# Kernel tuning notes

Measured on AMD Instinct MI355X. Metric: run time of the kernel, lower is better.

The kernel has to match this reference:

```python
import jax, jax.numpy as jnp
import numpy as np

N, T, D, H, P = 4096, 365, 16, 256, 2


def setup_inputs() -> dict:
    key = jax.random.key(0)
    ks = jax.random.split(key, 16)
    std = 0.02
    inputs = jax.random.normal(ks[0], (N, T, D), dtype=jnp.float32)
    A = jax.random.uniform(ks[1], (N, N), dtype=jnp.float32)
    A = A / jnp.sum(A, axis=1, keepdims=True)  # row-normalized adjacency
    return {
        "inputs": inputs,
        "A": A,
        # Keras LSTMCell params: kernel [D,4H], recurrent_kernel [H,4H], bias [4H]
        "kernel": jax.random.normal(ks[2], (D, 4 * H), dtype=jnp.float32) * std,
        "rkernel": jax.random.normal(ks[3], (H, 4 * H), dtype=jnp.float32) * std,
        "lstm_bias": jnp.zeros((4 * H,), dtype=jnp.float32),
        "W_graph_h": jax.random.normal(ks[4], (H, H), dtype=jnp.float32) * std,
        "b_graph_h": jnp.zeros((H,), dtype=jnp.float32),
        "W_graph_c": jax.random.normal(ks[5], (H, H), dtype=jnp.float32) * std,
        "b_graph_c": jnp.zeros((H,), dtype=jnp.float32),
        "W_h_cur": jax.random.normal(ks[6], (H, H), dtype=jnp.float32) * std,
        "W_h_prev": jax.random.normal(ks[7], (H, H), dtype=jnp.float32) * std,
        "b_h": jnp.zeros((H,), dtype=jnp.float32),
        "W_c_cur": jax.random.normal(ks[8], (H, H), dtype=jnp.float32) * std,
        "W_c_prev": jax.random.normal(ks[9], (H, H), dtype=jnp.float32) * std,
        "b_c": jnp.zeros((H,), dtype=jnp.float32),
        "W_out": jax.random.normal(ks[10], (H, P), dtype=jnp.float32) * std,
        "b_out": jnp.zeros((P,), dtype=jnp.float32),
    }


def reference(inputs, A, kernel, rkernel, lstm_bias,
              W_graph_h, b_graph_h, W_graph_c, b_graph_c,
              W_h_cur, W_h_prev, b_h, W_c_cur, W_c_prev, b_c,
              W_out, b_out):
    h = A.shape[0] and None  # noop; shapes: inputs [N,T,D]
    n = A.shape[0]
    hs = W_graph_h.shape[0]

    def step(carry, x_t):
        h_prev, c_prev = carry  # [N,H] each
        # graph propagation of previous states
        h_graph = jnp.tanh(A @ (h_prev @ W_graph_h + b_graph_h))
        c_graph = jnp.tanh(A @ (c_prev @ W_graph_c + b_graph_c))
        # Keras LSTMCell (gate order i, f, g, o)
        z = x_t @ kernel + h_prev @ rkernel + lstm_bias  # [N,4H]
        zi, zf, zg, zo = jnp.split(z, 4, axis=-1)
        c_cur = jax.nn.sigmoid(zf) * c_prev + jax.nn.sigmoid(zi) * jnp.tanh(zg)
        h_cur = jax.nn.sigmoid(zo) * jnp.tanh(c_cur)
        # gated merge of LSTM state and graph-propagated state
        h_update = jax.nn.sigmoid(h_cur @ W_h_cur + h_graph @ W_h_prev + b_h)
        c_update = jax.nn.sigmoid(c_cur @ W_c_cur + c_graph @ W_c_prev + b_c)
        out_pred = h_update @ W_out + b_out  # [N,P]
        return (h_update, c_update), out_pred

    init = (jnp.zeros((n, hs), dtype=inputs.dtype),
            jnp.zeros((n, hs), dtype=inputs.dtype))
    xs = jnp.swapaxes(inputs, 0, 1)  # [T,N,D]
    _, outs = jax.lax.scan(step, init, xs)  # [T,N,P]
    return jnp.swapaxes(outs, 0, 1)  # [N,T,P]
```

## Files before the change

### kernel.cpp

```cpp
#include <hip/hip_runtime.h>

using short8 = __attribute__((ext_vector_type(8))) short;
using f32x4  = __attribute__((ext_vector_type(4))) float;

#define NN 4096
#define TT 365
#define DD 16
#define HH 256
#define PP 2
#define TD (TT*DD)
#define TP (TT*PP)
#define KG 320
#define ASCALE 4096.0f
#define HWSCALE 64.0f
#define AINV2 (1.0f/(4096.0f*64.0f))

__device__ __forceinline__ unsigned short f2bf(float f) {
    union { float f; unsigned u; } v; v.f = f;
    unsigned r = v.u + 0x7FFFu + ((v.u >> 16) & 1u);
    return (unsigned short)(r >> 16);
}
__device__ __forceinline__ unsigned char f2e4m3(float f) {
    union { float f; unsigned u; } v; v.f = f;
    unsigned s = (v.u >> 24) & 0x80u;
    unsigned au = v.u & 0x7fffffffu;
    if (au >= 0x43E00000u) return (unsigned char)(s | 0x7E);
    if (au < 0x3C800000u) {
        int m = __float2int_rn(__uint_as_float(au) * 512.0f);
        return (unsigned char)(s | (unsigned)m);
    }
    unsigned r = au + 0x7FFFFu + ((au >> 20) & 1u);
    return (unsigned char)(s | ((r >> 20) - 0x3C0u));
}
__device__ __forceinline__ float sigmoidf_(float x) {
    return 1.0f / (1.0f + __expf(-x));
}
__device__ __forceinline__ float tanhf_(float x) {
    float t = __expf(2.0f * x);
    return (t - 1.0f) / (t + 1.0f);
}
__device__ __forceinline__ void async16(const void* g, void* l) {
    __builtin_amdgcn_global_load_lds(
        (const __attribute__((address_space(1))) void*)g,
        (__attribute__((address_space(3))) void*)l, 16, 0, 0);
}

template<int TI>
__device__ __forceinline__ void gemm_core_db(
    const unsigned short* __restrict__ Amat, int lda,
    const unsigned short* __restrict__ Bt,  int ldb,
    int k_len, int row0, int col0,
    unsigned short* As, unsigned short* Bs,
    f32x4 (&acc)[TI][4])
{
    const int tid  = threadIdx.x;
    const int lane = tid & 63;
    const int wave = tid >> 6;
    const int srow = lane >> 3;
    const int sblk = lane & 7;
    const int ABUF = TI * 32 * 64;
    const int BBUF = 128 * 64;

    const unsigned short* Ag = Amat + (size_t)(row0 + wave*8 + srow) * lda
                                    + ((sblk ^ srow) * 8);
    const unsigned short* Bg = Bt   + (size_t)(col0 + wave*8 + srow) * ldb
                                    + ((sblk ^ srow) * 8);

    const int fr = lane & 15;
    const int fq = lane >> 4;
    const int wr = (wave >> 1) * (TI * 16);
    const int wc = (wave & 1) * 64;
    const int off0 = ((fq ^ (fr & 7)) * 8);

    {
        unsigned short* AsW = As + wave * 512;
        unsigned short* BsW = Bs + wave * 512;
        #pragma unroll
        for (int q = 0; q < TI; q++) async16(Ag + (size_t)q * 32 * lda, AsW + q * 2048);
        #pragma unroll
        for (int q = 0; q < 4;  q++) async16(Bg + (size_t)q * 32 * ldb, BsW + q * 2048);
    }
    asm volatile("s_waitcnt vmcnt(0)" ::: "memory");
    __syncthreads();

    const int nk = k_len >> 6;
    int sel = 0;
    for (int it = 0; it < nk; ++it) {
        if (it + 1 < nk) {
            const unsigned short* Agn = Ag + (it + 1) * 64;
            const unsigned short* Bgn = Bg + (it + 1) * 64;
            unsigned short* AsW = As + (sel ^ 1) * ABUF + wave * 512;
            unsigned short* BsW = Bs + (sel ^ 1) * BBUF + wave * 512;
            #pragma unroll
            for (int q = 0; q < TI; q++) async16(Agn + (size_t)q * 32 * lda, AsW + q * 2048);
            #pragma unroll
            for (int q = 0; q < 4;  q++) async16(Bgn + (size_t)q * 32 * ldb, BsW + q * 2048);
        }
        const unsigned short* Ab = As + sel * ABUF;
        const unsigned short* Bb = Bs + sel * BBUF;
        #pragma unroll
        for (int kh = 0; kh < 2; kh++) {
            const int off = off0 ^ (kh * 32);
            short8 a[TI], b[4];
            #pragma unroll
            for (int i = 0; i < TI; i++)
                a[i] = *(const short8*)(Ab + (wr + i*16 + fr) * 64 + off);
            #pragma unroll
            for (int j = 0; j < 4;  j++)
                b[j] = *(const short8*)(Bb + (wc + j*16 + fr) * 64 + off);
            #pragma unroll
            for (int i = 0; i < TI; i++)
                #pragma unroll
                for (int j = 0; j < 4; j++)
                    acc[i][j] = __builtin_amdgcn_mfma_f32_16x16x32_bf16(
                        a[i], b[j], acc[i][j], 0, 0, 0);
        }
        asm volatile("s_waitcnt vmcnt(0)" ::: "memory");
        __syncthreads();
        sel ^= 1;
    }
}

template<int TI>
__device__ __forceinline__ void gemm8_db(
    const unsigned char* __restrict__ Amat,
    const unsigned char* __restrict__ Bmat,
    int kb, int klen, int row0, int col0,
    unsigned char* As, unsigned char* Bs,
    f32x4 (&acc)[TI][4])
{
    const int tid  = threadIdx.x;
    const int lane = tid & 63;
    const int wave = tid >> 6;
    const int srow = lane >> 3;
    const int sblk = lane & 7;
    const int ABUF = TI * 32 * 128;
    const int BBUF = 128 * 128;

    const unsigned char* Ag = Amat + (size_t)(row0 + wave*8 + srow) * NN
                                   + ((sblk ^ srow) * 16) + kb;
    const unsigned char* Bg = Bmat + (size_t)(col0 + wave*8 + srow) * NN
                                   + ((sblk ^ srow) * 16) + kb;

    const int fr = lane & 15;
    const int fq = lane >> 4;
    const int wr = (wave >> 1) * (TI * 16);
    const int wc = (wave & 1) * 64;
    int offk[4];
    #pragma unroll
    for (int kq = 0; kq < 4; kq++)
        offk[kq] = (((kq*2 + (fq >> 1)) ^ (fr & 7)) << 4) + ((fq & 1) << 3);

    {
        unsigned char* AsW = As + wave * 1024;
        unsigned char* BsW = Bs + wave * 1024;
        #pragma unroll
        for (int q = 0; q < TI; q++) async16(Ag + (size_t)q * 32 * NN, AsW + q * 4096);
        #pragma unroll
        for (int q = 0; q < 4;  q++) async16(Bg + (size_t)q * 32 * NN, BsW + q * 4096);
    }
    asm volatile("s_waitcnt vmcnt(0)" ::: "memory");
    __syncthreads();

    const int nk = klen >> 7;
    int sel = 0;
    for (int it = 0; it < nk; ++it) {
        if (it + 1 < nk) {
            const unsigned char* Agn = Ag + (size_t)(it + 1) * 128;
            const unsigned char* Bgn = Bg + (size_t)(it + 1) * 128;
            unsigned char* AsW = As + (sel ^ 1) * ABUF + wave * 1024;
            unsigned char* BsW = Bs + (sel ^ 1) * BBUF + wave * 1024;
            #pragma unroll
            for (int q = 0; q < TI; q++) async16(Agn + (size_t)q * 32 * NN, AsW + q * 4096);
            #pragma unroll
            for (int q = 0; q < 4;  q++) async16(Bgn + (size_t)q * 32 * NN, BsW + q * 4096);
        }
        const unsigned char* Ab = As + sel * ABUF;
        const unsigned char* Bb = Bs + sel * BBUF;
        #pragma unroll
        for (int kq = 0; kq < 4; kq++) {
            long a[TI], b[4];
            #pragma unroll
            for (int i = 0; i < TI; i++) a[i] = *(const long*)(Ab + (wr + i*16 + fr) * 128 + offk[kq]);
            #pragma unroll
            for (int j = 0; j < 4;  j++) b[j] = *(const long*)(Bb + (wc + j*16 + fr) * 128 + offk[kq]);
            #pragma unroll
            for (int i = 0; i < TI; i++)
                #pragma unroll
                for (int j = 0; j < 4; j++)
                    acc[i][j] = __builtin_amdgcn_mfma_f32_16x16x32_fp8_fp8(
                        a[i], b[j], acc[i][j], 0, 0, 0);
        }
        asm volatile("s_waitcnt vmcnt(0)" ::: "memory");
        __syncthreads();
        sel ^= 1;
    }
}


__global__ __launch_bounds__(256) void k_prep_a(const float* __restrict__ A,
                                                unsigned char* __restrict__ A8) {
    size_t i = (size_t)blockIdx.x * blockDim.x + threadIdx.x;
    size_t stride = (size_t)gridDim.x * blockDim.x;
    size_t total = (size_t)NN * NN / 4;
    for (; i < total; i += stride) {
        float4 v = ((const float4*)A)[i];
        unsigned pk = (unsigned)f2e4m3(v.x * ASCALE)
                    | ((unsigned)f2e4m3(v.y * ASCALE) << 8)
                    | ((unsigned)f2e4m3(v.z * ASCALE) << 16)
                    | ((unsigned)f2e4m3(v.w * ASCALE) << 24);
        ((unsigned*)A8)[i] = pk;
    }
}

__global__ __launch_bounds__(256) void k_prep_w(
    const float* __restrict__ Wgh, const float* __restrict__ Wgc,
    const float* __restrict__ rk,  const float* __restrict__ kern,
    const float* __restrict__ lb,
    const float* __restrict__ Whc, const float* __restrict__ Whp,
    const float* __restrict__ Wcc, const float* __restrict__ Wcp,
    unsigned short* __restrict__ WzTb, unsigned short* __restrict__ WgT,
    unsigned short* __restrict__ WU, float* __restrict__ biasg)
{
    int i = blockIdx.x * blockDim.x + threadIdx.x;
    int stride = gridDim.x * blockDim.x;
    for (int x = i; x < 1024 * KG; x += stride) {
        int col = x / KG, k = x % KG;
        int oc = (((col >> 4) & 3) << 8) + ((col >> 6) << 4) + (col & 15);
        float val = 0.f;
        if (k < 256) val = rk[k * 1024 + oc];
        else if (k < 272) val = kern[(k - 256) * 1024 + oc];
        WzTb[x] = f2bf(val);
    }
    for (int x = i; x < 512 * 256; x += stride) {
        int col = x >> 8, k = x & 255;
        float val = (col < 256) ? Wgh[k * 256 + col] : Wgc[k * 256 + (col - 256)];
        WgT[x] = f2bf(val);
    }
    for (int x = i; x < 512 * 512; x += stride) {
        int col = x >> 9, k = x & 511;
        float val;
        if (col < 256)
            val = (k < 256) ? Whc[k * 256 + col] : Whp[(k - 256) * 256 + col];
        else {
            int c2 = col - 256;
            val = (k < 256) ? Wcc[k * 256 + c2] : Wcp[(k - 256) * 256 + c2];
        }
        WU[x] = f2bf(val);
    }
    for (int x = i; x < 1024; x += stride)
        biasg[x] = lb[(((x >> 4) & 3) << 8) + ((x >> 6) << 4) + (x & 15)];
}

__global__ __launch_bounds__(256) void k_prep_s(const float* __restrict__ inputs,
                                                unsigned short* __restrict__ HCb,
                                                unsigned char* __restrict__ hwT8,
                                                float* __restrict__ Cstate)
{
    int i = blockIdx.x * blockDim.x + threadIdx.x;
    int stride = gridDim.x * blockDim.x;
    for (int x = i; x < NN * KG; x += stride) {
        int n = x / KG, col = x % KG;
        unsigned short v = 0;
        if (col >= 256 && col < 272)
            v = f2bf(inputs[(size_t)n * TD + (col - 256)]);
        HCb[x] = v;
    }
    for (int x = i; x < 512 * NN / 4; x += stride) ((unsigned*)hwT8)[x] = 0;
    for (int x = i; x < NN * HH; x += stride) Cstate[x] = 0.f;
}


__global__ __launch_bounds__(256, 2) void k_a(
    const unsigned char* __restrict__ A8,
    const unsigned char* __restrict__ hwT8,
    const float* __restrict__ bgh, const float* __restrict__ bgc,
    const unsigned short* __restrict__ HCb,
    const unsigned short* __restrict__ WzTb,
    const float* __restrict__ biasg,
    const float* __restrict__ Cstate,
    unsigned short* __restrict__ LHS3)
{
    __shared__ __align__(16) unsigned char smem[65536];
    const int bid = blockIdx.x;
    const int tid = threadIdx.x;
    const int lane = tid & 63;
    const int wave = tid >> 6;
    const int fr = lane & 15;
    const int rq = (lane >> 4) * 4;

    if (bid < 256) {
        const int x  = bid & 7;
        const int q  = bid >> 3;
        const int row0 = (x * 8 + (q & 7)) * 64;
        const int col0 = (q >> 3) * 128;
        f32x4 acc[2][4] = {};
        gemm8_db<2>(A8, hwT8, 0, NN, row0, col0, smem, smem + 16384, acc);
        const int wr = (wave >> 1) * 32;
        const int wc = (wave & 1) * 64;
        #pragma unroll
        for (int i = 0; i < 2; i++)
            #pragma unroll
            for (int j = 0; j < 4; j++) {
                int c = col0 + wc + j * 16 + fr;
                float bias = (c < 256) ? bgh[c] : bgc[c - 256];
                int dst = (c < 256) ? (c + 256) : (c + 512);
                int rbase = row0 + wr + i * 16 + rq;
                #pragma unroll
                for (int r = 0; r < 4; r++)
                    LHS3[(size_t)(rbase + r) * 1024 + dst] =
                        f2bf(tanhf_(acc[i][j][r] * AINV2 + bias));
            }
    } else {
        const int b2 = bid - 256;
        f32x4 acc[4][4] = {};
        const int row0 = (b2 >> 3) * 128;
        const int col0 = (b2 & 7) * 128;
        gemm_core_db<4>(HCb, KG, WzTb, KG, KG, row0, col0,
                        (unsigned short*)smem, (unsigned short*)(smem + 32768), acc);
        const int wr = (wave >> 1) * 64, wc = (wave & 1) * 64;
        const int h = (((col0 + wc) >> 6) << 4) + fr;
        float bgv[4];
        #pragma unroll
        for (int j = 0; j < 4; j++) bgv[j] = biasg[col0 + wc + j * 16 + fr];
        #pragma unroll
        for (int i = 0; i < 4; i++) {
            const int rbase = row0 + wr + i * 16 + rq;
            #pragma unroll
            for (int r = 0; r < 4; r++) {
                const int n = rbase + r;
                float z_i = acc[i][0][r] + bgv[0];
                float z_f = acc[i][1][r] + bgv[1];
                float z_g = acc[i][2][r] + bgv[2];
                float z_o = acc[i][3][r] + bgv[3];
                float cp = Cstate[n * HH + h];
                float ccur = sigmoidf_(z_f) * cp + sigmoidf_(z_i) * tanhf_(z_g);
                float hcur = sigmoidf_(z_o) * tanhf_(ccur);
                LHS3[(size_t)n * 1024 + h] = f2bf(hcur);
                LHS3[(size_t)n * 1024 + 512 + h] = f2bf(ccur);
            }
        }
    }
}

__global__ __launch_bounds__(256, 2) void k_uf(
    const unsigned short* __restrict__ LHS3,
    const unsigned short* __restrict__ WU,
    const unsigned short* __restrict__ WgT,
    const float* __restrict__ b_h, const float* __restrict__ b_c,
    const float* __restrict__ W_out, const float* __restrict__ b_out,
    float* __restrict__ Cstate,
    unsigned short* __restrict__ HCb,
    unsigned char* __restrict__ hwT8,
    float* __restrict__ d_out,
    const float* __restrict__ inputs, int t)
{
    __shared__ __align__(16) unsigned char smem[74752];
    unsigned short* As  = (unsigned short*)smem;
    unsigned short* Bs  = (unsigned short*)(smem + 8192);
    unsigned short* Us  = (unsigned short*)smem;
    unsigned short* B2s = (unsigned short*)(smem + 16384);
    float* outred = (float*)(smem + 73728);

    const int bid  = blockIdx.x;
    const int tid  = threadIdx.x;
    const int lane = tid & 63;
    const int wave = tid >> 6;
    const int fr   = lane & 15;
    const int fq   = lane >> 4;
    const int rq   = fq * 4;
    const int srow = lane >> 3;
    const int sblk = lane & 7;

    const int half = bid & 1;
    const int row0 = (bid >> 1) * 16;
    const int wc   = wave * 64;
    const int off0 = ((fq ^ (fr & 7)) * 8);
    const int ABUF = 1024, BBUF = 16384;

    const unsigned short* Ag = LHS3 + half*512
        + (size_t)(row0 + wave*8 + srow) * 1024 + ((sblk ^ srow) * 8);
    const unsigned short* Bg = WU
        + (size_t)(half*256 + wave*64 + srow) * 512 + ((sblk ^ srow) * 8);

    if (wave < 2) async16(Ag, As + wave*512);
    #pragma unroll
    for (int q = 0; q < 8; q++)
        async16(Bg + (size_t)q*8*512, Bs + wave*4096 + q*512);
    asm volatile("s_waitcnt vmcnt(0)" ::: "memory");
    __syncthreads();

    f32x4 acc[4] = {};
    int sel = 0;
    for (int it = 0; it < 8; ++it) {
        const int nit = it + 1;
        if (nit < 8) {
            if (wave < 2) async16(Ag + nit*64, As + (sel^1)*ABUF + wave*512);
            #pragma unroll
            for (int q = 0; q < 8; q++)
                async16(Bg + nit*64 + (size_t)q*8*512,
                        Bs + (sel^1)*BBUF + wave*4096 + q*512);
        }
        const unsigned short* Ab = As + sel*ABUF;
        const unsigned short* Bb = Bs + sel*BBUF;
        #pragma unroll
        for (int kh2 = 0; kh2 < 2; kh2++) {
            const int off = off0 ^ (kh2 * 32);
            short8 a = *(const short8*)(Ab + fr * 64 + off);
            short8 b[4];
            #pragma unroll
            for (int j = 0; j < 4; j++)
                b[j] = *(const short8*)(Bb + (wc + j*16 + fr) * 64 + off);
            #pragma unroll
            for (int j = 0; j < 4; j++)
                acc[j] = __builtin_amdgcn_mfma_f32_16x16x32_bf16(
                    a, b[j], acc[j], 0, 0, 0);
        }
        asm volatile("s_waitcnt vmcnt(0)" ::: "memory");
        __syncthreads();
        sel ^= 1;
    }

    const float* bias = half ? b_c : b_h;
    float pr0[4], pr1[4];
    #pragma unroll
    for (int m = 0; m < 4; m++) { pr0[m] = 0.f; pr1[m] = 0.f; }
    #pragma unroll
    for (int j = 0; j < 4; j++) {
        const int cl = wc + j*16 + fr;
        const float bv = bias[cl];
        const int blk = j*2 + (fr >> 3);
        float w0 = 0.f, w1 = 0.f;
        if (half == 0) { w0 = W_out[cl*2 + 0]; w1 = W_out[cl*2 + 1]; }
        #pragma unroll
        for (int r = 0; r < 4; r++) {
            const int rl = rq + r;
            const int n = row0 + rl;
            float v = sigmoidf_(acc[j][r] + bv);
            unsigned short vb = f2bf(v);
            Us[rl*256 + wave*64 + ((blk ^ (rl & 7)) * 8) + (fr & 7)] = vb;
            if (half == 0) {
                HCb[(size_t)n * KG + cl] = vb;
                pr0[r] += v * w0;
                pr1[r] += v * w1;
            } else {
                Cstate[(size_t)n * HH + cl] = v;
            }
        }
    }
    if (half == 0) {
        #pragma unroll
        for (int m = 0; m < 4; m++) {
            #pragma unroll
            for (int s = 1; s < 16; s <<= 1) {
                pr0[m] += __shfl_xor(pr0[m], s, 64);
                pr1[m] += __shfl_xor(pr1[m], s, 64);
            }
        }
        if (fr == 0) {
            #pragma unroll
            for (int r = 0; r < 4; r++) {
                int rl = rq + r;
                outred[(wave*16 + rl)*2 + 0] = pr0[r];
                outred[(wave*16 + rl)*2 + 1] = pr1[r];
            }
        }
    }
    __syncthreads();
    if (half == 0 && tid < 32) {
        int rl = tid >> 1, p = tid & 1;
        float s = b_out[p];
        #pragma unroll
        for (int w = 0; w < 4; w++) s += outred[(w*16 + rl)*2 + p];
        d_out[(size_t)(row0 + rl) * TP + t * PP + p] = s;
    }

    f32x4 acc2[4] = {};
    const unsigned short* Bg2 = WgT
        + (size_t)(half*256 + wave*64 + srow) * 256 + ((sblk ^ srow) * 8);
    for (int kc2 = 0; kc2 < 4; ++kc2) {
        __syncthreads();
        #pragma unroll
        for (int q = 0; q < 8; q++)
            async16(Bg2 + (size_t)q*8*256 + kc2*64, B2s + wave*4096 + q*512);
        asm volatile("s_waitcnt vmcnt(0)" ::: "memory");
        __syncthreads();
        #pragma unroll
        for (int kh2 = 0; kh2 < 2; kh2++) {
            const int off = off0 ^ (kh2 * 32);
            short8 a = *(const short8*)(Us + fr * 256 + kc2*64 + off);
            short8 b[4];
            #pragma unroll
            for (int j = 0; j < 4; j++)
                b[j] = *(const short8*)(B2s + (wc + j*16 + fr) * 64 + off);
            #pragma unroll
            for (int j = 0; j < 4; j++)
                acc2[j] = __builtin_amdgcn_mfma_f32_16x16x32_bf16(
                    a, b[j], acc2[j], 0, 0, 0);
        }
    }
    unsigned pk[4];
    #pragma unroll
    for (int j = 0; j < 4; j++)
        pk[j] = (unsigned)f2e4m3(acc2[j][0] * HWSCALE)
              | ((unsigned)f2e4m3(acc2[j][1] * HWSCALE) << 8)
              | ((unsigned)f2e4m3(acc2[j][2] * HWSCALE) << 16)
              | ((unsigned)f2e4m3(acc2[j][3] * HWSCALE) << 24);
    unsigned o0 = 0, o1 = 0, o2 = 0, o3 = 0;
    #pragma unroll
    for (int d = 0; d < 4; d++) {
        unsigned g0 = __shfl(pk[d],  0 + fr, 64);
        unsigned g1 = __shfl(pk[d], 16 + fr, 64);
        unsigned g2 = __shfl(pk[d], 32 + fr, 64);
        unsigned g3 = __shfl(pk[d], 48 + fr, 64);
        if (fq == d) { o0 = g0; o1 = g1; o2 = g2; o3 = g3; }
    }
    {
        int cg = half*256 + wc + fq*16 + fr;
        uint4 o; o.x = o0; o.y = o1; o.z = o2; o.w = o3;
        *(uint4*)(hwT8 + (size_t)cg * NN + row0) = o;
    }

    if (half == 0 && t + 1 < TT) {
        int gid = (bid >> 1) * 256 + tid;
        int n = gid >> 4, d = gid & 15;
        HCb[(size_t)n * KG + 256 + d] = f2bf(inputs[(size_t)n * TD + (t + 1) * DD + d]);
    }
}

extern "C" void kernel_launch(void* const* d_in, const int* in_sizes, int n_in,
                              void* d_out_v, int out_size, void* d_ws, size_t ws_size,
                              hipStream_t stream)
{
    const float* inputs = (const float*)d_in[0];
    const float* A      = (const float*)d_in[1];
    const float* kern   = (const float*)d_in[2];
    const float* rk     = (const float*)d_in[3];
    const float* lb     = (const float*)d_in[4];
    const float* Wgh    = (const float*)d_in[5];
    const float* bgh    = (const float*)d_in[6];
    const float* Wgc    = (const float*)d_in[7];
    const float* bgc    = (const float*)d_in[8];
    const float* Whc    = (const float*)d_in[9];
    const float* Whp    = (const float*)d_in[10];
    const float* bh     = (const float*)d_in[11];
    const float* Wcc    = (const float*)d_in[12];
    const float* Wcp    = (const float*)d_in[13];
    const float* bc     = (const float*)d_in[14];
    const float* Wout   = (const float*)d_in[15];
    const float* bout   = (const float*)d_in[16];
    float* d_out = (float*)d_out_v;

    char* ws = (char*)d_ws;
    size_t off = 0;
    auto alloc = [&](size_t bytes) {
        char* p = ws + off;
        off += (bytes + 255) & ~(size_t)255;
        return p;
    };
    unsigned char*  A8    = (unsigned char*) alloc((size_t)NN * NN);
    unsigned char*  hwT8  = (unsigned char*) alloc((size_t)512 * NN);
    unsigned short* HCb   = (unsigned short*)alloc((size_t)NN * KG * 2);
    unsigned short* WzTb  = (unsigned short*)alloc((size_t)1024 * KG * 2);
    unsigned short* WgT   = (unsigned short*)alloc((size_t)512 * 256 * 2);
    unsigned short* WU    = (unsigned short*)alloc((size_t)512 * 512 * 2);
    float*          biasg = (float*)         alloc(1024 * 4);
    unsigned short* LHS3  = (unsigned short*)alloc((size_t)NN * 1024 * 2);
    float*          Cst   = (float*)         alloc((size_t)NN * HH * 4);
    (void)in_sizes; (void)n_in; (void)out_size; (void)ws_size;

    k_prep_a<<<2048, 256, 0, stream>>>(A, A8);
    k_prep_w<<<256, 256, 0, stream>>>(Wgh, Wgc, rk, kern, lb,
                                      Whc, Whp, Wcc, Wcp, WzTb, WgT, WU, biasg);
    k_prep_s<<<512, 256, 0, stream>>>(inputs, HCb, hwT8, Cst);

    for (int t = 0; t < TT; t++) {
        k_a<<<512, 256, 0, stream>>>(A8, hwT8, bgh, bgc,
                                     HCb, WzTb, biasg, Cst, LHS3);
        k_uf<<<512, 256, 0, stream>>>(LHS3, WU, WgT, bh, bc, Wout, bout,
                                      Cst, HCb, hwT8, d_out, inputs, t);
    }
}
```

Measured before the change: 16.01 ms.

## Use partial vmcnt waits and raw barriers to overlap prefetch with MFMA

```diff
diff --git a/kernel.cpp b/kernel.cpp
--- a/kernel.cpp
+++ b/kernel.cpp
@@ -80,8 +80,6 @@
         #pragma unroll
         for (int q = 0; q < 4;  q++) async16(Bg + (size_t)q * 32 * ldb, BsW + q * 2048);
     }
-    asm volatile("s_waitcnt vmcnt(0)" ::: "memory");
-    __syncthreads();
 
     const int nk = k_len >> 6;
     int sel = 0;
@@ -95,7 +93,14 @@
             for (int q = 0; q < TI; q++) async16(Agn + (size_t)q * 32 * lda, AsW + q * 2048);
             #pragma unroll
             for (int q = 0; q < 4;  q++) async16(Bgn + (size_t)q * 32 * ldb, BsW + q * 2048);
-        }
+            if constexpr (TI == 4)      asm volatile("s_waitcnt vmcnt(8)" ::: "memory");
+            else if constexpr (TI == 2) asm volatile("s_waitcnt vmcnt(6)" ::: "memory");
+            else                        asm volatile("s_waitcnt vmcnt(0)" ::: "memory");
+        } else {
+            asm volatile("s_waitcnt vmcnt(0)" ::: "memory");
+        }
+        __builtin_amdgcn_s_barrier();
+        __builtin_amdgcn_sched_barrier(0);
         const unsigned short* Ab = As + sel * ABUF;
         const unsigned short* Bb = Bs + sel * BBUF;
         #pragma unroll
@@ -115,8 +120,7 @@
                     acc[i][j] = __builtin_amdgcn_mfma_f32_16x16x32_bf16(
                         a[i], b[j], acc[i][j], 0, 0, 0);
         }
-        asm volatile("s_waitcnt vmcnt(0)" ::: "memory");
-        __syncthreads();
+        __builtin_amdgcn_s_barrier();
         sel ^= 1;
     }
 }
@@ -159,8 +163,6 @@
         #pragma unroll
         for (int q = 0; q < 4;  q++) async16(Bg + (size_t)q * 32 * NN, BsW + q * 4096);
     }
-    asm volatile("s_waitcnt vmcnt(0)" ::: "memory");
-    __syncthreads();
 
     const int nk = klen >> 7;
     int sel = 0;
@@ -174,7 +176,14 @@
             for (int q = 0; q < TI; q++) async16(Agn + (size_t)q * 32 * NN, AsW + q * 4096);
             #pragma unroll
             for (int q = 0; q < 4;  q++) async16(Bgn + (size_t)q * 32 * NN, BsW + q * 4096);
-        }
+            if constexpr (TI == 4)      asm volatile("s_waitcnt vmcnt(8)" ::: "memory");
+            else if constexpr (TI == 2) asm volatile("s_waitcnt vmcnt(6)" ::: "memory");
+            else                        asm volatile("s_waitcnt vmcnt(0)" ::: "memory");
+        } else {
+            asm volatile("s_waitcnt vmcnt(0)" ::: "memory");
+        }
+        __builtin_amdgcn_s_barrier();
+        __builtin_amdgcn_sched_barrier(0);
         const unsigned char* Ab = As + sel * ABUF;
         const unsigned char* Bb = Bs + sel * BBUF;
         #pragma unroll
@@ -191,8 +200,7 @@
                     acc[i][j] = __builtin_amdgcn_mfma_f32_16x16x32_fp8_fp8(
                         a[i], b[j], acc[i][j], 0, 0, 0);
         }
-        asm volatile("s_waitcnt vmcnt(0)" ::: "memory");
-        __syncthreads();
+        __builtin_amdgcn_s_barrier();
         sel ^= 1;
     }
 }
@@ -359,7 +367,7 @@
     unsigned short* As  = (unsigned short*)smem;
     unsigned short* Bs  = (unsigned short*)(smem + 8192);
     unsigned short* Us  = (unsigned short*)smem;
-    unsigned short* B2s = (unsigned short*)(smem + 16384);
+    unsigned short* B2s = (unsigned short*)(smem + 8192);
     float* outred = (float*)(smem + 73728);
 
     const int bid  = blockIdx.x;
@@ -387,8 +395,6 @@
     #pragma unroll
     for (int q = 0; q < 8; q++)
         async16(Bg + (size_t)q*8*512, Bs + wave*4096 + q*512);
-    asm volatile("s_waitcnt vmcnt(0)" ::: "memory");
-    __syncthreads();
 
     f32x4 acc[4] = {};
     int sel = 0;
@@ -400,7 +406,13 @@
             for (int q = 0; q < 8; q++)
                 async16(Bg + nit*64 + (size_t)q*8*512,
                         Bs + (sel^1)*BBUF + wave*4096 + q*512);
-        }
+            if (wave < 2) asm volatile("s_waitcnt vmcnt(9)" ::: "memory");
+            else          asm volatile("s_waitcnt vmcnt(8)" ::: "memory");
+        } else {
+            asm volatile("s_waitcnt vmcnt(0)" ::: "memory");
+        }
+        __builtin_amdgcn_s_barrier();
+        __builtin_amdgcn_sched_barrier(0);
         const unsigned short* Ab = As + sel*ABUF;
         const unsigned short* Bb = Bs + sel*BBUF;
         #pragma unroll
@@ -416,8 +428,7 @@
                 acc[j] = __builtin_amdgcn_mfma_f32_16x16x32_bf16(
                     a, b[j], acc[j], 0, 0, 0);
         }
-        asm volatile("s_waitcnt vmcnt(0)" ::: "memory");
-        __syncthreads();
+        __builtin_amdgcn_s_barrier();
         sel ^= 1;
     }
 
@@ -478,13 +489,23 @@
     f32x4 acc2[4] = {};
     const unsigned short* Bg2 = WgT
         + (size_t)(half*256 + wave*64 + srow) * 256 + ((sblk ^ srow) * 8);
+    #pragma unroll
+    for (int q = 0; q < 8; q++)
+        async16(Bg2 + (size_t)q*8*256, B2s + wave*4096 + q*512);
+    int sel2 = 0;
     for (int kc2 = 0; kc2 < 4; ++kc2) {
-        __syncthreads();
-        #pragma unroll
-        for (int q = 0; q < 8; q++)
-            async16(Bg2 + (size_t)q*8*256 + kc2*64, B2s + wave*4096 + q*512);
-        asm volatile("s_waitcnt vmcnt(0)" ::: "memory");
-        __syncthreads();
+        if (kc2 + 1 < 4) {
+            #pragma unroll
+            for (int q = 0; q < 8; q++)
+                async16(Bg2 + (size_t)q*8*256 + (kc2+1)*64,
+                        B2s + (sel2^1)*BBUF + wave*4096 + q*512);
+            asm volatile("s_waitcnt vmcnt(8)" ::: "memory");
+        } else {
+            asm volatile("s_waitcnt vmcnt(0)" ::: "memory");
+        }
+        __builtin_amdgcn_s_barrier();
+        __builtin_amdgcn_sched_barrier(0);
+        const unsigned short* Bb2 = B2s + sel2*BBUF;
         #pragma unroll
         for (int kh2 = 0; kh2 < 2; kh2++) {
             const int off = off0 ^ (kh2 * 32);
@@ -492,12 +513,14 @@
             short8 b[4];
             #pragma unroll
             for (int j = 0; j < 4; j++)
-                b[j] = *(const short8*)(B2s + (wc + j*16 + fr) * 64 + off);
+                b[j] = *(const short8*)(Bb2 + (wc + j*16 + fr) * 64 + off);
             #pragma unroll
             for (int j = 0; j < 4; j++)
                 acc2[j] = __builtin_amdgcn_mfma_f32_16x16x32_bf16(
                     a, b[j], acc2[j], 0, 0, 0);
         }
+        __builtin_amdgcn_s_barrier();
+        sel2 ^= 1;
     }
     unsigned pk[4];
     #pragma unroll
```

Measured after the change: 15.49 ms. 1.03x faster.
